# Kernel tuning notes

Measured on AMD Instinct MI355X. Metric: run time of the kernel, lower is better.

The kernel has to match this reference:

```python
import jax, jax.numpy as jnp
import numpy as np

MARGIN = 1.0

def setup_inputs() -> dict:
    key = jax.random.key(0)
    k1, k2, k3 = jax.random.split(key, 3)
    B, C, D = 65536, 1000, 512
    x = jax.random.normal(k1, (B, D), dtype=jnp.float32)
    x = x / jnp.linalg.norm(x, axis=1, keepdims=True)  # docstring: ||x||2 = 1
    labels = jax.random.randint(k2, (B,), 0, C, dtype=jnp.int64)
    centers = jax.random.normal(k3, (C, D), dtype=jnp.float32)
    return {"x": x, "labels": labels, "centers": centers}

def reference(x, labels, centers):
    # l2Norm applied to the centers (module is only used when l2Norm is truthy)
    c = centers / jnp.linalg.norm(centers, axis=1, keepdims=True)  # (C, D)
    # cosine distance to every center: one batched GEMM instead of per-sample loop
    dist = 1.0 - jnp.einsum("bd,cd->bc", x, c)                      # (B, C)
    pos = jnp.take_along_axis(dist, labels[:, None], axis=1)[:, 0]  # (B,)
    # min over all classes != label: mask own class with +inf
    same = jnp.arange(c.shape[0])[None, :] == labels[:, None]       # (B, C)
    neg = jnp.min(jnp.where(same, jnp.inf, dist), axis=1)           # (B,)
    # sum of per-sample hinge losses divided by batch size == mean
    return jnp.mean(jax.nn.relu(pos + MARGIN - neg))
```

## Files before the change

kernel.cpp:

```cpp
#include <hip/hip_runtime.h>
#include <stdint.h>

typedef short v8s __attribute__((ext_vector_type(8)));
typedef short v4s __attribute__((ext_vector_type(4)));
typedef float v4f __attribute__((ext_vector_type(4)));

#define BM 128
#define BN 128
#define BK 64
#define LDT 72

#define POS_INF __builtin_inff()

__device__ __forceinline__ short f2bf(float f) {
    uint32_t u = __builtin_bit_cast(uint32_t, f);
    u += 0x7fffu + ((u >> 16) & 1u);
    return (short)(u >> 16);
}

__global__ void prep_centers(const float* __restrict__ centers,
                             unsigned short* __restrict__ cbf,
                             int C, int D, float* __restrict__ out) {
    const int row  = blockIdx.x;
    const int lane = threadIdx.x;
    if (row == 0 && lane == 0) out[0] = 0.0f;
    if (row >= C) {
        v4s z = {0, 0, 0, 0};
        for (int d = lane * 4; d < D; d += 256)
            *(v4s*)&cbf[(size_t)row * D + d] = z;
        return;
    }
    const float* src = centers + (size_t)row * D;
    float ss = 0.0f;
    for (int d = lane * 4; d < D; d += 256) {
        v4f f = *(const v4f*)&src[d];
        ss += f.x * f.x + f.y * f.y + f.z * f.z + f.w * f.w;
    }
    #pragma unroll
    for (int off = 32; off; off >>= 1) ss += __shfl_xor(ss, off, 64);
    const float rn = rsqrtf(ss);
    for (int d = lane * 4; d < D; d += 256) {
        v4f f = *(const v4f*)&src[d];
        v4s s;
        s.x = f2bf(f.x * rn); s.y = f2bf(f.y * rn);
        s.z = f2bf(f.z * rn); s.w = f2bf(f.w * rn);
        *(v4s*)&cbf[(size_t)row * D + d] = s;
    }
}

__global__ void convert_x(const float* __restrict__ x,
                          unsigned short* __restrict__ xbf, size_t n) {
    size_t i = ((size_t)blockIdx.x * blockDim.x + threadIdx.x) * 8;
    if (i >= n) return;
    v4f f0 = *(const v4f*)&x[i];
    v4f f1 = *(const v4f*)&x[i + 4];
    v8s s;
    s[0] = f2bf(f0.x); s[1] = f2bf(f0.y); s[2] = f2bf(f0.z); s[3] = f2bf(f0.w);
    s[4] = f2bf(f1.x); s[5] = f2bf(f1.y); s[6] = f2bf(f1.z); s[7] = f2bf(f1.w);
    *(v8s*)&xbf[i] = s;
}

__global__ void gemm_fused(const float* __restrict__ xf,
                           const unsigned short* __restrict__ xbf, int useBf,
                           const unsigned short* __restrict__ cbf,
                           const int* __restrict__ labels,
                           float* __restrict__ pos, float* __restrict__ partial,
                           int Bt, int C, int D, int NT) {
    __shared__ short As[BM * LDT];
    __shared__ short Bs[BN * LDT];
    __shared__ int   Ls[BM];
    __shared__ float sMinW[2][BM];

    const int t    = threadIdx.x;
    const int row0 = blockIdx.x * BM;
    const int nt   = blockIdx.y;
    const int n0   = nt * BN;

    if (t < BM) Ls[t] = labels[row0 + t];

    const int lane = t & 63;
    const int wave = t >> 6;
    const int wm = wave >> 1, wn = wave & 1;
    const int l15 = lane & 15, q = lane >> 4;

    v4f acc[4][4];
    #pragma unroll
    for (int i = 0; i < 4; ++i)
        #pragma unroll
        for (int j = 0; j < 4; ++j)
            acc[i][j] = (v4f){0.f, 0.f, 0.f, 0.f};

    const int KT = D / BK;
    for (int kk = 0; kk < KT; ++kk) {
        const int k0 = kk * BK;
        #pragma unroll
        for (int p = 0; p < 4; ++p) {
            int r = (t >> 3) + p * 32;
            int ch = t & 7;
            v8s v = *(const v8s*)&cbf[(size_t)(n0 + r) * D + k0 + ch * 8];
            *(v8s*)&Bs[r * LDT + ch * 8] = v;
        }
        if (useBf) {
            #pragma unroll
            for (int p = 0; p < 4; ++p) {
                int r = (t >> 3) + p * 32;
                int ch = t & 7;
                v8s v = *(const v8s*)&xbf[(size_t)(row0 + r) * D + k0 + ch * 8];
                *(v8s*)&As[r * LDT + ch * 8] = v;
            }
        } else {
            #pragma unroll
            for (int p = 0; p < 8; ++p) {
                int r = (t >> 4) + p * 16;
                int c4 = t & 15;
                v4f f = *(const v4f*)&xf[(size_t)(row0 + r) * D + k0 + c4 * 4];
                v4s s;
                s.x = f2bf(f.x); s.y = f2bf(f.y);
                s.z = f2bf(f.z); s.w = f2bf(f.w);
                *(v4s*)&As[r * LDT + c4 * 4] = s;
            }
        }
        __syncthreads();
        #pragma unroll
        for (int ki = 0; ki < BK; ki += 32) {
            v8s a[4], b[4];
            #pragma unroll
            for (int i = 0; i < 4; ++i)
                a[i] = *(const v8s*)&As[(wm * 64 + i * 16 + l15) * LDT + ki + q * 8];
            #pragma unroll
            for (int j = 0; j < 4; ++j)
                b[j] = *(const v8s*)&Bs[(wn * 64 + j * 16 + l15) * LDT + ki + q * 8];
            #pragma unroll
            for (int i = 0; i < 4; ++i)
                #pragma unroll
                for (int j = 0; j < 4; ++j)
                    acc[i][j] = __builtin_amdgcn_mfma_f32_16x16x32_bf16(
                        a[i], b[j], acc[i][j], 0, 0, 0);
        }
        __syncthreads();
    }

    #pragma unroll
    for (int i = 0; i < 4; ++i) {
        #pragma unroll
        for (int rg = 0; rg < 4; ++rg) {
            const int row_l = wm * 64 + i * 16 + q * 4 + rg;
            const int lab = Ls[row_l];
            float m = POS_INF;
            #pragma unroll
            for (int j = 0; j < 4; ++j) {
                const int col = n0 + wn * 64 + j * 16 + l15;
                const float d = 1.0f - acc[i][j][rg];
                if (col == lab) pos[row0 + row_l] = d;
                else if (col < C) m = fminf(m, d);
            }
            m = fminf(m, __shfl_xor(m, 1, 64));
            m = fminf(m, __shfl_xor(m, 2, 64));
            m = fminf(m, __shfl_xor(m, 4, 64));
            m = fminf(m, __shfl_xor(m, 8, 64));
            if (l15 == 0) sMinW[wn][row_l] = m;
        }
    }
    __syncthreads();
    if (t < BM) {
        const float m = fminf(sMinW[0][t], sMinW[1][t]);
        partial[(size_t)nt * Bt + row0 + t] = m;
    }
}

__global__ void reduce_loss(const float* __restrict__ pos,
                            const float* __restrict__ partial,
                            int Bt, int NT, float margin,
                            float* __restrict__ out) {
    const int r = blockIdx.x * 256 + threadIdx.x;
    float h = 0.0f;
    if (r < Bt) {
        float neg = POS_INF;
        for (int tt = 0; tt < NT; ++tt)
            neg = fminf(neg, partial[(size_t)tt * Bt + r]);
        h = fmaxf(0.0f, pos[r] + margin - neg);
    }
    #pragma unroll
    for (int off = 32; off; off >>= 1) h += __shfl_down(h, off, 64);
    __shared__ float wsum[4];
    const int lane = threadIdx.x & 63, wave = threadIdx.x >> 6;
    if (lane == 0) wsum[wave] = h;
    __syncthreads();
    if (threadIdx.x == 0)
        atomicAdd(out, (wsum[0] + wsum[1] + wsum[2] + wsum[3]) * (1.0f / (float)Bt));
}

extern "C" void kernel_launch(void* const* d_in, const int* in_sizes, int n_in,
                              void* d_out, int out_size, void* d_ws, size_t ws_size,
                              hipStream_t stream) {
    const float* x       = (const float*)d_in[0];
    const int*   labels  = (const int*)d_in[1];
    const float* centers = (const float*)d_in[2];
    float* out = (float*)d_out;

    const int Bt = in_sizes[1];
    const int D  = in_sizes[0] / Bt;
    const int C  = in_sizes[2] / D;
    const int NT = (C + BN - 1) / BN;
    const int CP = NT * BN;

    char* ws = (char*)d_ws;
    unsigned short* cbf = (unsigned short*)ws;
    size_t off = (size_t)CP * D * 2;
    off = (off + 255) & ~(size_t)255;
    float* pos = (float*)(ws + off);      off += (size_t)Bt * 4;
    float* partial = (float*)(ws + off);  off += (size_t)NT * Bt * 4;
    unsigned short* xbf = (unsigned short*)(ws + off);
    const size_t needBig = off + (size_t)Bt * D * 2;
    const int useBf = (ws_size >= needBig) ? 1 : 0;

    prep_centers<<<CP, 64, 0, stream>>>(centers, cbf, C, D, out);
    if (useBf) {
        const size_t n = (size_t)Bt * D;
        convert_x<<<(unsigned)((n / 8 + 255) / 256), 256, 0, stream>>>(x, xbf, n);
    }
    dim3 grid(Bt / BM, NT);
    gemm_fused<<<grid, 256, 0, stream>>>(x, xbf, useBf, cbf, labels, pos, partial,
                                         Bt, C, D, NT);
    reduce_loss<<<(Bt + 255) / 256, 256, 0, stream>>>(pos, partial, Bt, NT, 1.0f, out);
}
```

Measured before the change: 335.5 us.

## Load GEMM tiles directly into LDS with XOR-swizzled layout and swap grid order

Replaces register-staged global-to-LDS copies with global_load_lds direct transfers, and drops the padded LDS row stride in favour of an XOR swizzle on 16-byte chunks so MFMA fragment reads avoid bank conflicts. The grid is transposed so consecutive blocks share the same x row tile across center tiles, improving L2 reuse of x. This frees VGPRs and issue slots used for copying, but relies on the direct-to-LDS builtin's per-wave contiguous placement matching the swizzle math.

```diff
diff --git a/kernel.cpp b/kernel.cpp
--- a/kernel.cpp
+++ b/kernel.cpp
@@ -8,9 +8,14 @@
 #define BM 128
 #define BN 128
 #define BK 64
-#define LDT 72
-
 #define POS_INF __builtin_inff()
+
+typedef __attribute__((address_space(3))) unsigned int lds_uint;
+typedef const __attribute__((address_space(1))) unsigned int glb_uint;
+
+__device__ __forceinline__ void load16_lds(const void* g, void* l) {
+    __builtin_amdgcn_global_load_lds((glb_uint*)g, (lds_uint*)l, 16, 0, 0);
+}
 
 __device__ __forceinline__ short f2bf(float f) {
     uint32_t u = __builtin_bit_cast(uint32_t, f);
@@ -66,14 +71,14 @@
                            const int* __restrict__ labels,
                            float* __restrict__ pos, float* __restrict__ partial,
                            int Bt, int C, int D, int NT) {
-    __shared__ short As[BM * LDT];
-    __shared__ short Bs[BN * LDT];
+    __shared__ short As[BM * BK];
+    __shared__ short Bs[BN * BK];
     __shared__ int   Ls[BM];
     __shared__ float sMinW[2][BM];
 
     const int t    = threadIdx.x;
-    const int row0 = blockIdx.x * BM;
-    const int nt   = blockIdx.y;
+    const int nt   = blockIdx.x;
+    const int row0 = blockIdx.y * BM;
     const int n0   = nt * BN;
 
     if (t < BM) Ls[t] = labels[row0 + t];
@@ -83,6 +88,9 @@
     const int wm = wave >> 1, wn = wave & 1;
     const int l15 = lane & 15, q = lane >> 4;
 
+    const int rsub = lane >> 3;
+    const int csrc = (lane & 7) ^ rsub;
+
     v4f acc[4][4];
     #pragma unroll
     for (int i = 0; i < 4; ++i)
@@ -95,41 +103,50 @@
         const int k0 = kk * BK;
         #pragma unroll
         for (int p = 0; p < 4; ++p) {
-            int r = (t >> 3) + p * 32;
-            int ch = t & 7;
-            v8s v = *(const v8s*)&cbf[(size_t)(n0 + r) * D + k0 + ch * 8];
-            *(v8s*)&Bs[r * LDT + ch * 8] = v;
+            const int rbase = wave * 32 + p * 8;
+            const unsigned short* g =
+                &cbf[(size_t)(n0 + rbase + rsub) * D + k0 + csrc * 8];
+            load16_lds(g, &Bs[rbase * BK]);
         }
         if (useBf) {
             #pragma unroll
             for (int p = 0; p < 4; ++p) {
-                int r = (t >> 3) + p * 32;
-                int ch = t & 7;
-                v8s v = *(const v8s*)&xbf[(size_t)(row0 + r) * D + k0 + ch * 8];
-                *(v8s*)&As[r * LDT + ch * 8] = v;
+                const int rbase = wave * 32 + p * 8;
+                const unsigned short* g =
+                    &xbf[(size_t)(row0 + rbase + rsub) * D + k0 + csrc * 8];
+                load16_lds(g, &As[rbase * BK]);
             }
         } else {
             #pragma unroll
-            for (int p = 0; p < 8; ++p) {
-                int r = (t >> 4) + p * 16;
-                int c4 = t & 15;
-                v4f f = *(const v4f*)&xf[(size_t)(row0 + r) * D + k0 + c4 * 4];
-                v4s s;
-                s.x = f2bf(f.x); s.y = f2bf(f.y);
-                s.z = f2bf(f.z); s.w = f2bf(f.w);
-                *(v4s*)&As[r * LDT + c4 * 4] = s;
+            for (int p = 0; p < 4; ++p) {
+                const int r = (t >> 3) + p * 32;
+                const int cs = t & 7;
+                const float* src = &xf[(size_t)(row0 + r) * D + k0 + cs * 8];
+                v4f f0 = *(const v4f*)&src[0];
+                v4f f1 = *(const v4f*)&src[4];
+                v8s s;
+                s[0] = f2bf(f0.x); s[1] = f2bf(f0.y);
+                s[2] = f2bf(f0.z); s[3] = f2bf(f0.w);
+                s[4] = f2bf(f1.x); s[5] = f2bf(f1.y);
+                s[6] = f2bf(f1.z); s[7] = f2bf(f1.w);
+                *(v8s*)&As[r * BK + (cs ^ (r & 7)) * 8] = s;
             }
         }
         __syncthreads();
         #pragma unroll
         for (int ki = 0; ki < BK; ki += 32) {
+            const int cbase = ki >> 3;
             v8s a[4], b[4];
             #pragma unroll
-            for (int i = 0; i < 4; ++i)
-                a[i] = *(const v8s*)&As[(wm * 64 + i * 16 + l15) * LDT + ki + q * 8];
-            #pragma unroll
-            for (int j = 0; j < 4; ++j)
-                b[j] = *(const v8s*)&Bs[(wn * 64 + j * 16 + l15) * LDT + ki + q * 8];
+            for (int i = 0; i < 4; ++i) {
+                const int m = wm * 64 + i * 16 + l15;
+                a[i] = *(const v8s*)&As[m * BK + (((cbase + q) ^ (l15 & 7)) * 8)];
+            }
+            #pragma unroll
+            for (int j = 0; j < 4; ++j) {
+                const int n = wn * 64 + j * 16 + l15;
+                b[j] = *(const v8s*)&Bs[n * BK + (((cbase + q) ^ (l15 & 7)) * 8)];
+            }
             #pragma unroll
             for (int i = 0; i < 4; ++i)
                 #pragma unroll
@@ -219,7 +236,7 @@
         const size_t n = (size_t)Bt * D;
         convert_x<<<(unsigned)((n / 8 + 255) / 256), 256, 0, stream>>>(x, xbf, n);
     }
-    dim3 grid(Bt / BM, NT);
+    dim3 grid(NT, Bt / BM);
     gemm_fused<<<grid, 256, 0, stream>>>(x, xbf, useBf, cbf, labels, pos, partial,
                                          Bt, C, D, NT);
     reduce_loss<<<(Bt + 255) / 256, 256, 0, stream>>>(pos, partial, Bt, NT, 1.0f, out);
```

Measured after the change: 298.5 us. -11.0%, faster.
